# Optimization experiments

Measured on AMD Instinct MI355X. Metric: run time of the kernel, lower is better.

Reference implementation:

```python
import jax, jax.numpy as jnp
import numpy as np

N, NB, NP, T = 1024, 16, 256, 80
EPS_LEN = 1e-9   # seg_len clamp_min in original
EPS_DD = 1e-12   # dot(d,d) clamp_min in original


def setup_inputs() -> dict:
    key = jax.random.key(0)
    k1, k2, k3, k4 = jax.random.split(key, 4)
    # smooth-ish random trajectory (cumsum of steps)
    selected_traj = jnp.cumsum(jax.random.normal(k1, (N, T, 3), jnp.float32) * 0.5, axis=1)
    # random polylines per (sample, boundary)
    road_points = jnp.cumsum(jax.random.normal(k2, (N, NB, NP, 3), jnp.float32) * 0.5, axis=2) \
                  + jax.random.normal(k3, (N, NB, 1, 3), jnp.float32) * 2.0
    # ragged valid-prefix masks, length in [2, NP]
    lengths = jax.random.randint(k4, (N, NB), 2, NP + 1)
    road_mask = jnp.arange(NP)[None, None, :] < lengths[:, :, None]
    return {"selected_traj": selected_traj, "road_points": road_points, "road_mask": road_mask}


def _arc_project(pos, rp, rm):
    # pos: [N,T,3]; rp: [N,NB,NP,3]; rm: [N,NB,NP] bool
    n, t = pos.shape[0], pos.shape[1]
    nb, npts = rp.shape[1], rp.shape[2]
    inf = jnp.asarray(jnp.inf, pos.dtype)
    ar = jnp.arange(npts)
    n_valid = rm.sum(-1)                                    # [N,NB]

    # pack valid points to the front, preserving order (== boolean-mask gather in torch)
    order = jnp.argsort(jnp.logical_not(rm), axis=-1, stable=True)
    pts_f = jnp.take_along_axis(rp, order[..., None], axis=2)      # [N,NB,NP,3]
    pack_mask = ar[None, None, :] < n_valid[:, :, None]
    pts_f = jnp.where(pack_mask[..., None], pts_f, 0.0)
    # flipped direction: reverse the valid prefix
    flip_idx = jnp.clip(n_valid[:, :, None] - 1 - ar[None, None, :], 0, npts - 1)
    pts_b = jnp.take_along_axis(pts_f, flip_idx[..., None], axis=2)
    pts_b = jnp.where(pack_mask[..., None], pts_b, 0.0)
    pts = jnp.stack([pts_f, pts_b], axis=2)                 # [N,NB,2,NP,3]

    # segment i is real iff i < n_valid-1
    seg_mask = ar[: npts - 1][None, None, None, :] < (n_valid - 1)[:, :, None, None]  # [N,NB,1,NP-1]
    seg_vec = pts[..., 1:, :] - pts[..., :-1, :]            # [N,NB,2,NP-1,3]
    seg_norm = jnp.sqrt((seg_vec ** 2).sum(-1))
    seg_len = jnp.where(seg_mask, jnp.maximum(seg_norm, EPS_LEN), 0.0)
    cum_s = jnp.concatenate([jnp.zeros_like(seg_len[..., :1]), jnp.cumsum(seg_len, -1)], -1)  # [N,NB,2,NP]
    last_idx = jnp.clip(n_valid - 1, 0, npts - 1)[:, :, None, None]
    total_s = jnp.take_along_axis(cum_s, jnp.broadcast_to(last_idx, (n, nb, 2, 1)), -1)  # [N,NB,2,1]

    # entry: project first trajectory point onto nearest valid segment
    p0 = pos[:, 0][:, None, None, None, :]                  # [N,1,1,1,3]
    a0 = pts[..., :-1, :]
    dd0 = jnp.maximum((seg_vec ** 2).sum(-1), EPS_DD)
    t0 = jnp.clip(((p0 - a0) * seg_vec).sum(-1) / dd0, 0.0, 1.0)
    q0 = a0 + t0[..., None] * seg_vec
    d2 = jnp.where(seg_mask, ((p0 - q0) ** 2).sum(-1), inf)
    seg0 = jnp.argmin(d2, -1)[..., None]                    # [N,NB,2,1]
    entry_s = jnp.take_along_axis(cum_s, seg0, -1) + jnp.take_along_axis(t0 * seg_len, seg0, -1)

    # trajectory arc-length, resample polyline at entry_s + traj arc length
    traj_seg = jnp.sqrt(((pos[:, 1:] - pos[:, :-1]) ** 2).sum(-1))
    traj_cs = jnp.concatenate([jnp.zeros_like(traj_seg[:, :1]), jnp.cumsum(traj_seg, -1)], -1)  # [N,T]
    target_s = jnp.clip(entry_s + traj_cs[:, None, None, :], 0.0, total_s)  # [N,NB,2,T]

    j = jax.vmap(lambda c, tg: jnp.searchsorted(c, tg, side='right'))(
        cum_s.reshape(-1, npts), target_s.reshape(-1, t)) - 1
    j = jnp.clip(j.reshape(n, nb, 2, t), 0, jnp.maximum(n_valid[:, :, None, None] - 2, 0))

    seg_l = jnp.take_along_axis(seg_len, j, -1)
    cs_j = jnp.take_along_axis(cum_s, j, -1)
    t_loc = jnp.clip((target_s - cs_j) / jnp.maximum(seg_l, EPS_LEN), 0.0, 1.0)
    pa = jnp.take_along_axis(pts, j[..., None], axis=3)
    pb = jnp.take_along_axis(pts, (j + 1)[..., None], axis=3)
    proj = pa + t_loc[..., None] * (pb - pa)                # [N,NB,2,T,3]

    # pick (boundary, direction) candidate with min total L2 cost
    cost = jnp.sqrt(((pos[:, None, None] - proj) ** 2).sum(-1)).sum(-1)  # [N,NB,2]
    cand_ok = (n_valid >= 2)[:, :, None]
    cost = jnp.where(cand_ok, cost, inf)
    best = jnp.argmin(cost.reshape(n, -1), -1)
    best_proj = jnp.take_along_axis(proj.reshape(n, -1, t, 3), best[:, None, None, None], axis=1)[:, 0]
    has = cand_ok.any((1, 2))
    return jnp.where(has[:, None, None], best_proj, pos)


def reference(selected_traj, road_points, road_mask):
    pos = selected_traj[..., 0:3]
    out_pos = _arc_project(pos, road_points, road_mask)
    return jnp.concatenate([out_pos, selected_traj[..., 3:]], axis=-1)
```

## Files before the change

kernel.cpp:

```cpp
#include <hip/hip_runtime.h>
#include <math.h>

#define NN 1024
#define NBB 16
#define NP 256
#define TT 80
#define EPS_LEN 1e-9f
#define EPS_DD 1e-12f

__device__ __forceinline__ float frcp(float x){ return __builtin_amdgcn_rcpf(x); }
__device__ __forceinline__ float fsq(float x){ return __builtin_amdgcn_sqrtf(x); }
__device__ __forceinline__ float rfl_f(float x){
  return __builtin_bit_cast(float, __builtin_amdgcn_readfirstlane(__builtin_bit_cast(int, x)));
}
__device__ __forceinline__ float rlane_f(float x, int l){
  return __builtin_bit_cast(float, __builtin_amdgcn_readlane(__builtin_bit_cast(int, x), l));
}

template<int CTRL,int RM>
__device__ __forceinline__ float dpp_add(float v){
  int t = __builtin_amdgcn_update_dpp(0, __builtin_bit_cast(int, v), CTRL, RM, 0xf, true);
  return v + __builtin_bit_cast(float, t);
}
__device__ __forceinline__ float wave_incl_scan(float v){
  v = dpp_add<0x111,0xf>(v);
  v = dpp_add<0x112,0xf>(v);
  v = dpp_add<0x114,0xf>(v);
  v = dpp_add<0x118,0xf>(v);
  v = dpp_add<0x142,0xa>(v);
  v = dpp_add<0x143,0xc>(v);
  return v;
}
template<int CTRL,int RM>
__device__ __forceinline__ float dpp_min(float v){
  int t = __builtin_amdgcn_update_dpp(0x7f800000, __builtin_bit_cast(int,v), CTRL, RM, 0xf, false);
  return fminf(v, __builtin_bit_cast(float,t));
}
__device__ __forceinline__ float wave_min_all(float v){
  v=dpp_min<0x111,0xf>(v); v=dpp_min<0x112,0xf>(v);
  v=dpp_min<0x114,0xf>(v); v=dpp_min<0x118,0xf>(v);
  v=dpp_min<0x142,0xa>(v); v=dpp_min<0x143,0xc>(v);
  return rlane_f(v, 63);
}

__device__ __forceinline__ void lds_fence() {
  __builtin_amdgcn_wave_barrier();
  asm volatile("s_waitcnt lgkmcnt(0)" ::: "memory");
  __builtin_amdgcn_wave_barrier();
}

__device__ __forceinline__ int wave_nv(const void* mask, size_t base, int lane) {
  bool as_byte = ((const unsigned char*)mask)[1] != 0;
  int nv = 0;
  if (as_byte) {
    uchar4 v = ((const uchar4*)((const unsigned char*)mask + base))[lane];
    nv += __popcll(__ballot(v.x != 0));
    nv += __popcll(__ballot(v.y != 0));
    nv += __popcll(__ballot(v.z != 0));
    nv += __popcll(__ballot(v.w != 0));
  } else {
    int4 v = ((const int4*)((const int*)mask + base))[lane];
    nv += __popcll(__ballot(v.x != 0));
    nv += __popcll(__ballot(v.y != 0));
    nv += __popcll(__ballot(v.z != 0));
    nv += __popcll(__ballot(v.w != 0));
  }
  return nv;
}

template<bool STRICT>
__device__ __forceinline__ int count256(const float* __restrict__ cs,
                                        const float* co, float v){
  int K = 0;
  #pragma unroll
  for (int k=0;k<16;k++) K += STRICT ? (co[k] < v) : (co[k] <= v);
  int base = (K < 16 ? K : 15) * 16;
  const float4* f4 = (const float4*)(cs + base);
  float4 c0=f4[0], c1=f4[1], c2=f4[2], c3=f4[3];
  int r;
  if (STRICT)
    r = (c0.x<v)+(c0.y<v)+(c0.z<v)+(c0.w<v)+(c1.x<v)+(c1.y<v)+(c1.z<v)+(c1.w<v)
      + (c2.x<v)+(c2.y<v)+(c2.z<v)+(c2.w<v)+(c3.x<v)+(c3.y<v)+(c3.z<v)+(c3.w<v);
  else
    r = (c0.x<=v)+(c0.y<=v)+(c0.z<=v)+(c0.w<=v)+(c1.x<=v)+(c1.y<=v)+(c1.z<=v)+(c1.w<=v)
      + (c2.x<=v)+(c2.y<=v)+(c2.z<=v)+(c2.w<=v)+(c3.x<=v)+(c3.y<=v)+(c3.z<=v)+(c3.w<=v);
  return (K >= 16) ? 256 : (base + r);
}

struct SegOut {
  float cpre[4];
  float run;
  float bdf, btf; int bjf;
  float bdl, btl; int bjl;
};

__device__ __forceinline__ void seg_pass(const float4* __restrict__ p4, int lane, int nv,
                                         float p0x, float p0y, float p0z,
                                         float* __restrict__ px, float* __restrict__ py,
                                         float* __restrict__ pz, SegOut& R) {
  const int j0 = lane * 4;
  float4 A = make_float4(0.f,0.f,0.f,0.f), B = A, C = A;
  if (j0 < nv) { A = p4[lane*3+0]; B = p4[lane*3+1]; C = p4[lane*3+2]; }
  float x[5], y[5], z[5];
  x[0]=A.x; y[0]=A.y; z[0]=A.z;
  x[1]=A.w; y[1]=B.x; z[1]=B.y;
  x[2]=B.z; y[2]=B.w; z[2]=C.x;
  x[3]=C.y; y[3]=C.z; z[3]=C.w;
  x[4]=__shfl_down(x[0],1,64); y[4]=__shfl_down(y[0],1,64); z[4]=__shfl_down(z[0],1,64);
  ((float4*)px)[lane] = make_float4(x[0],x[1],x[2],x[3]);
  ((float4*)py)[lane] = make_float4(y[0],y[1],y[2],y[3]);
  ((float4*)pz)[lane] = make_float4(z[0],z[1],z[2],z[3]);
  float run = 0.f;
  R.bdf=INFINITY; R.btf=0.f; R.bjf=j0;
  R.bdl=INFINITY; R.btl=0.f; R.bjl=j0;
  #pragma unroll
  for (int k=0;k<4;k++){
    bool valid = (j0+k) < nv-1;
    float vx=x[k+1]-x[k], vy=y[k+1]-y[k], vz=z[k+1]-z[k];
    float n2 = vx*vx+vy*vy+vz*vz;
    float sl = valid ? fmaxf(fsq(n2), EPS_LEN) : 0.f;
    float t = ((p0x-x[k])*vx+(p0y-y[k])*vy+(p0z-z[k])*vz) * frcp(fmaxf(n2,EPS_DD));
    t = fminf(fmaxf(t,0.f),1.f);
    float qx=x[k]+t*vx, qy=y[k]+t*vy, qz=z[k]+t*vz;
    float dx=p0x-qx, dy=p0y-qy, dz=p0z-qz;
    float d2 = valid ? (dx*dx+dy*dy+dz*dz) : INFINITY;
    if (d2 <  R.bdf){R.bdf=d2; R.bjf=j0+k; R.btf=t;}
    if (d2 <= R.bdl){R.bdl=d2; R.bjl=j0+k; R.btl=t;}
    run += sl; R.cpre[k]=run;
  }
  R.run = run;
}

template<int MODE>
__device__ void eval_wave(float* __restrict__ px, float* __restrict__ py,
                          float* __restrict__ pz, float* __restrict__ cs,
                          const float* __restrict__ pos, const float* __restrict__ tc,
                          const float4* __restrict__ p4, int nv,
                          float* __restrict__ cost2, int wdir, float* __restrict__ out) {
  const int lane = threadIdx.x & 63;
  SegOut R;
  seg_pass(p4, lane, nv, pos[0], pos[1], pos[2], px, py, pz, R);

  float inc = wave_incl_scan(R.run);
  float ex = inc - R.run;
  ((float4*)cs)[lane] = make_float4(ex, ex+R.cpre[0], ex+R.cpre[1], ex+R.cpre[2]);

  const float Tot = rlane_f(inc, 63);

  float cval = ex + R.cpre[2];
  float co[16];
  #pragma unroll
  for (int k=0;k<16;k++) co[k] = rfl_f(__shfl(cval, 4*k+3, 64));

  float minv = wave_min_all(R.bdf);
  unsigned long long mf = __ballot(R.bdf == minv);
  unsigned long long ml = __ballot(R.bdl == minv);
  int lf = __builtin_ctzll(mf);
  int ll = 63 - __builtin_clzll(ml);
  int   jf = __builtin_amdgcn_readlane(R.bjf, lf);
  float tf = rlane_f(R.btf, lf);
  int   jl = __builtin_amdgcn_readlane(R.bjl, ll);
  float tl0 = rlane_f(R.btl, ll);

  constexpr int NPASS = (MODE==0)?3:2;
  float l_tc[NPASS];
  #pragma unroll
  for (int p=0;p<NPASS;p++){
    int task = p*64 + lane;
    int r = (MODE==0 && task>=TT) ? task-TT : task;
    int t = (r < TT) ? r : 0;
    l_tc[p] = tc[t];
  }

  lds_fence();

  float csjf = cs[jf], csjf1 = cs[jf+1];
  float csjl = cs[jl], csjl1 = cs[jl+1];
  float e0 = csjf + tf*(csjf1-csjf);
  float e1 = (Tot - csjl1) + (1.f-tl0)*(csjl1-csjl);

  const int jmaxv = nv-2;
  float accf=0.f, accr=0.f;
  #pragma unroll
  for (int p=0;p<NPASS;p++){
    int task = p*64 + lane;
    int dir, t; bool act;
    if (MODE==0){ act = task<2*TT; dir = task>=TT?1:0; t = dir ? task-TT : task; }
    else        { act = task<TT;   dir = wdir;         t = task; }
    float ts = (dir ? e1 : e0) + l_tc[p];
    ts = fminf(fmaxf(ts,0.f),Tot);
    int ia, ib; float tl;
    if (dir){
      float v = Tot - ts;
      int lb = count256<true>(cs, co, v);
      int j = nv-1-lb; j = j<0?0:(j>jmaxv?jmaxv:j);
      int l2 = nv-1-j;
      float base = Tot - cs[l2];
      tl = (ts-base)*frcp(fmaxf(cs[l2]-cs[l2-1], EPS_LEN));
      ia=l2; ib=l2-1;
    } else {
      int ub = count256<false>(cs, co, ts);
      int j = ub-1; j = j<0?0:(j>jmaxv?jmaxv:j);
      tl = (ts - cs[j])*frcp(fmaxf(cs[j+1]-cs[j], EPS_LEN));
      ia=j; ib=j+1;
    }
    tl = fminf(fmaxf(tl,0.f),1.f);
    float ax=px[ia], ay=py[ia], az=pz[ia];
    float bx=px[ib], by=py[ib], bz=pz[ib];
    float prx=ax+tl*(bx-ax), pry=ay+tl*(by-ay), prz=az+tl*(bz-az);
    if (MODE==1){
      if (act){ out[t*3+0]=prx; out[t*3+1]=pry; out[t*3+2]=prz; }
    } else if (act){
      float dx=pos[t*3+0]-prx, dy=pos[t*3+1]-pry, dz=pos[t*3+2]-prz;
      float dd=fsq(dx*dx+dy*dy+dz*dz);
      if (dir) accr+=dd; else accf+=dd;
    }
  }
  if (MODE==0){
    #pragma unroll
    for (int d=1;d<64;d<<=1){ accf+=__shfl_xor(accf,d,64); accr+=__shfl_xor(accr,d,64); }
    if (lane==0){ cost2[0]=accf; cost2[1]=accr; }
  }
}

__global__ __launch_bounds__(256)
void traj_cs_kernel(const float* __restrict__ traj, float* __restrict__ tcs) {
  const int wid = threadIdx.x>>6, lane = threadIdx.x&63;
  const int n = blockIdx.x*4 + wid;
  const float* p = traj + (size_t)n*TT*3;
  float* o = tcs + (size_t)n*TT;
  float dx=p[(lane+1)*3+0]-p[lane*3+0];
  float dy=p[(lane+1)*3+1]-p[lane*3+1];
  float dz=p[(lane+1)*3+2]-p[lane*3+2];
  float sA = sqrtf(dx*dx+dy*dy+dz*dz);
  float incA = sA;
  #pragma unroll
  for (int d=1;d<64;d<<=1){ float ov=__shfl_up(incA,d,64); if(lane>=d) incA+=ov; }
  o[lane+1] = incA;
  float tot = __shfl(incA, 63, 64);
  float sB = 0.f;
  if (lane<15){
    int t = 64+lane;
    float ex=p[(t+1)*3+0]-p[t*3+0];
    float ey=p[(t+1)*3+1]-p[t*3+1];
    float ez=p[(t+1)*3+2]-p[t*3+2];
    sB = sqrtf(ex*ex+ey*ey+ez*ez);
  }
  float incB = sB;
  #pragma unroll
  for (int d=1;d<64;d<<=1){ float ov=__shfl_up(incB,d,64); if(lane>=d) incB+=ov; }
  if (lane<15) o[65+lane] = tot + incB;
  if (lane==0) o[0] = 0.f;
}

__global__ __launch_bounds__(256, 8)
void fused_cost_kernel(const float* __restrict__ traj, const float* __restrict__ rp,
                       const void* __restrict__ mask, const float* __restrict__ tcs,
                       float* __restrict__ cost) {
  __shared__ float s_px[4][NP], s_py[4][NP], s_pz[4][NP], s_cs[4][NP];
  const int wid = threadIdx.x>>6, lane = threadIdx.x&63;
  const int nb = blockIdx.x*4 + wid;
  const int n = nb / NBB;
  int nvr = wave_nv(mask, (size_t)nb*NP, lane);
  if (nvr < 2){
    if (lane==0){ cost[nb*2+0]=INFINITY; cost[nb*2+1]=INFINITY; }
    return;
  }
  eval_wave<0>(s_px[wid],s_py[wid],s_pz[wid],s_cs[wid],
               traj+(size_t)n*TT*3, tcs+(size_t)n*TT,
               (const float4*)(rp+(size_t)nb*NP*3), nvr,
               cost+(size_t)nb*2, 0, nullptr);
}

__global__ __launch_bounds__(256)
void winner_kernel(const float* __restrict__ traj, const float* __restrict__ rp,
                   const void* __restrict__ mask, const float* __restrict__ tcs,
                   const float* __restrict__ cost, float* __restrict__ out) {
  __shared__ float s_px[4][NP], s_py[4][NP], s_pz[4][NP], s_cs[4][NP];
  const int wid = threadIdx.x>>6, lane = threadIdx.x&63;
  const int n = blockIdx.x*4 + wid;
  const float* c = cost + (size_t)n*NBB*2;
  float bc = (lane<NBB*2) ? c[lane] : INFINITY;
  int bi = (lane<NBB*2) ? lane : 64;
  #pragma unroll
  for (int d=1;d<64;d<<=1){
    float oc=__shfl_xor(bc,d,64); int oi=__shfl_xor(bi,d,64);
    if (oc<bc || (oc==bc && oi<bi)){bc=oc;bi=oi;}
  }
  const float* pos = traj + (size_t)n*TT*3;
  float* o = out + (size_t)n*TT*3;
  if (bc == INFINITY){
    if (lane < 60) ((float4*)o)[lane] = ((const float4*)pos)[lane];
    return;
  }
  int b = bi>>1, dir = bi&1;
  const size_t nbi = (size_t)n*NBB + b;
  int nv = wave_nv(mask, nbi*NP, lane);
  nv = max(nv, 2);
  eval_wave<1>(s_px[wid],s_py[wid],s_pz[wid],s_cs[wid],
               pos, tcs+(size_t)n*TT,
               (const float4*)(rp+nbi*NP*3), nv, nullptr, dir, o);
}

extern "C" void kernel_launch(void* const* d_in, const int* in_sizes, int n_in,
                              void* d_out, int out_size, void* d_ws, size_t ws_size,
                              hipStream_t stream) {
  const float* traj = (const float*)d_in[0];
  const float* rp   = (const float*)d_in[1];
  const void*  mask = d_in[2];
  float* tcs  = (float*)d_ws;
  float* cost = tcs + (size_t)NN * TT;
  float* out  = (float*)d_out;

  hipLaunchKernelGGL(traj_cs_kernel, dim3(NN/4), dim3(256), 0, stream, traj, tcs);
  hipLaunchKernelGGL(fused_cost_kernel, dim3(NN*NBB/4), dim3(256), 0, stream,
                     traj, rp, mask, tcs, cost);
  hipLaunchKernelGGL(winner_kernel, dim3(NN/4), dim3(256), 0, stream,
                     traj, rp, mask, tcs, cost, out);
}
```

Baseline: 35.66 us.

## Store entry arc positions from cost pass and skip min search in winner

The cost kernel now writes each candidate's forward and reverse entry arc-lengths to workspace. The winner kernel reads them back instead of recomputing the closest-segment search, so its segment pass drops the min-distance work. Points are stored interleaved xyz in LDS so each endpoint lookup is one float3 load. The entry cumsum values come from registers via readlane rather than LDS, and readfirstlane-of-shuffle becomes a direct readlane. The cost is an extra workspace array plus small global writes and reads.

```diff
diff --git a/kernel.cpp b/kernel.cpp
--- a/kernel.cpp
+++ b/kernel.cpp
@@ -10,9 +10,6 @@
 
 __device__ __forceinline__ float frcp(float x){ return __builtin_amdgcn_rcpf(x); }
 __device__ __forceinline__ float fsq(float x){ return __builtin_amdgcn_sqrtf(x); }
-__device__ __forceinline__ float rfl_f(float x){
-  return __builtin_bit_cast(float, __builtin_amdgcn_readfirstlane(__builtin_bit_cast(int, x)));
-}
 __device__ __forceinline__ float rlane_f(float x, int l){
   return __builtin_bit_cast(float, __builtin_amdgcn_readlane(__builtin_bit_cast(int, x), l));
 }
@@ -31,6 +28,7 @@
   v = dpp_add<0x143,0xc>(v);
   return v;
 }
+__device__ __forceinline__ float wave_sum(float v){ return rlane_f(wave_incl_scan(v), 63); }
 template<int CTRL,int RM>
 __device__ __forceinline__ float dpp_min(float v){
   int t = __builtin_amdgcn_update_dpp(0x7f800000, __builtin_bit_cast(int,v), CTRL, RM, 0xf, false);
@@ -94,10 +92,10 @@
   float bdl, btl; int bjl;
 };
 
+template<bool NEEDMIN>
 __device__ __forceinline__ void seg_pass(const float4* __restrict__ p4, int lane, int nv,
                                          float p0x, float p0y, float p0z,
-                                         float* __restrict__ px, float* __restrict__ py,
-                                         float* __restrict__ pz, SegOut& R) {
+                                         float* __restrict__ pts, SegOut& R) {
   const int j0 = lane * 4;
   float4 A = make_float4(0.f,0.f,0.f,0.f), B = A, C = A;
   if (j0 < nv) { A = p4[lane*3+0]; B = p4[lane*3+1]; C = p4[lane*3+2]; }
@@ -107,9 +105,9 @@
   x[2]=B.z; y[2]=B.w; z[2]=C.x;
   x[3]=C.y; y[3]=C.z; z[3]=C.w;
   x[4]=__shfl_down(x[0],1,64); y[4]=__shfl_down(y[0],1,64); z[4]=__shfl_down(z[0],1,64);
-  ((float4*)px)[lane] = make_float4(x[0],x[1],x[2],x[3]);
-  ((float4*)py)[lane] = make_float4(y[0],y[1],y[2],y[3]);
-  ((float4*)pz)[lane] = make_float4(z[0],z[1],z[2],z[3]);
+  ((float4*)pts)[lane*3+0] = make_float4(x[0],y[0],z[0],x[1]);
+  ((float4*)pts)[lane*3+1] = make_float4(y[1],z[1],x[2],y[2]);
+  ((float4*)pts)[lane*3+2] = make_float4(z[2],x[3],y[3],z[3]);
   float run = 0.f;
   R.bdf=INFINITY; R.btf=0.f; R.bjf=j0;
   R.bdl=INFINITY; R.btl=0.f; R.bjl=j0;
@@ -119,38 +117,82 @@
     float vx=x[k+1]-x[k], vy=y[k+1]-y[k], vz=z[k+1]-z[k];
     float n2 = vx*vx+vy*vy+vz*vz;
     float sl = valid ? fmaxf(fsq(n2), EPS_LEN) : 0.f;
-    float t = ((p0x-x[k])*vx+(p0y-y[k])*vy+(p0z-z[k])*vz) * frcp(fmaxf(n2,EPS_DD));
-    t = fminf(fmaxf(t,0.f),1.f);
-    float qx=x[k]+t*vx, qy=y[k]+t*vy, qz=z[k]+t*vz;
-    float dx=p0x-qx, dy=p0y-qy, dz=p0z-qz;
-    float d2 = valid ? (dx*dx+dy*dy+dz*dz) : INFINITY;
-    if (d2 <  R.bdf){R.bdf=d2; R.bjf=j0+k; R.btf=t;}
-    if (d2 <= R.bdl){R.bdl=d2; R.bjl=j0+k; R.btl=t;}
+    if (NEEDMIN){
+      float t = ((p0x-x[k])*vx+(p0y-y[k])*vy+(p0z-z[k])*vz) * frcp(fmaxf(n2,EPS_DD));
+      t = fminf(fmaxf(t,0.f),1.f);
+      float qx=x[k]+t*vx, qy=y[k]+t*vy, qz=z[k]+t*vz;
+      float dx=p0x-qx, dy=p0y-qy, dz=p0z-qz;
+      float d2 = valid ? (dx*dx+dy*dy+dz*dz) : INFINITY;
+      if (d2 <  R.bdf){R.bdf=d2; R.bjf=j0+k; R.btf=t;}
+      if (d2 <= R.bdl){R.bdl=d2; R.bjl=j0+k; R.btl=t;}
+    }
     run += sl; R.cpre[k]=run;
   }
   R.run = run;
 }
 
-template<int MODE>
-__device__ void eval_wave(float* __restrict__ px, float* __restrict__ py,
-                          float* __restrict__ pz, float* __restrict__ cs,
-                          const float* __restrict__ pos, const float* __restrict__ tc,
-                          const float4* __restrict__ p4, int nv,
-                          float* __restrict__ cost2, int wdir, float* __restrict__ out) {
+__device__ __forceinline__ void cs_pair_from_regs(int idx, float ex, const SegOut& R,
+                                                  float& c0, float& c1){
+  int o = idx >> 2, r = idx & 3;
+  float a0 = (r==0)?0.f : (r==1)?R.cpre[0] : (r==2)?R.cpre[1] : R.cpre[2];
+  float a1 = (r==0)?R.cpre[0] : (r==1)?R.cpre[1] : (r==2)?R.cpre[2] : R.run;
+  c0 = rlane_f(ex + a0, o);
+  c1 = rlane_f(ex + a1, o);
+}
+
+__device__ __forceinline__ void interp_at(const float* __restrict__ pts,
+                                          const float* __restrict__ cs,
+                                          const float* co, float Tot, int nv, int jmaxv,
+                                          int dir, float ts,
+                                          float& prx, float& pry, float& prz){
+  int ia, ib; float tl;
+  if (dir){
+    float v = Tot - ts;
+    int lb = count256<true>(cs, co, v);
+    int j = nv-1-lb; j = j<0?0:(j>jmaxv?jmaxv:j);
+    int l2 = nv-1-j;
+    float base = Tot - cs[l2];
+    tl = (ts-base)*frcp(fmaxf(cs[l2]-cs[l2-1], EPS_LEN));
+    ia=l2; ib=l2-1;
+  } else {
+    int ub = count256<false>(cs, co, ts);
+    int j = ub-1; j = j<0?0:(j>jmaxv?jmaxv:j);
+    tl = (ts - cs[j])*frcp(fmaxf(cs[j+1]-cs[j], EPS_LEN));
+    ia=j; ib=j+1;
+  }
+  tl = fminf(fmaxf(tl,0.f),1.f);
+  float3 PA = *(const float3*)(pts + ia*3);
+  float3 PB = *(const float3*)(pts + ib*3);
+  prx = PA.x + tl*(PB.x-PA.x);
+  pry = PA.y + tl*(PB.y-PA.y);
+  prz = PA.z + tl*(PB.z-PA.z);
+}
+
+__device__ void eval_cost_wave(float* __restrict__ pts, float* __restrict__ cs,
+                               const float* __restrict__ pos, const float* __restrict__ tc,
+                               const float4* __restrict__ p4, int nv,
+                               float* __restrict__ cost2, float2* __restrict__ ent2){
   const int lane = threadIdx.x & 63;
+  float l_tc[3];
+  #pragma unroll
+  for (int p=0;p<3;p++){
+    int task = p*64 + lane;
+    int r = task>=TT ? task-TT : task;
+    int t = (r<TT) ? r : 0;
+    l_tc[p] = tc[t];
+  }
   SegOut R;
-  seg_pass(p4, lane, nv, pos[0], pos[1], pos[2], px, py, pz, R);
+  seg_pass<true>(p4, lane, nv, pos[0], pos[1], pos[2], pts, R);
 
   float inc = wave_incl_scan(R.run);
   float ex = inc - R.run;
   ((float4*)cs)[lane] = make_float4(ex, ex+R.cpre[0], ex+R.cpre[1], ex+R.cpre[2]);
-
   const float Tot = rlane_f(inc, 63);
 
   float cval = ex + R.cpre[2];
   float co[16];
   #pragma unroll
-  for (int k=0;k<16;k++) co[k] = rfl_f(__shfl(cval, 4*k+3, 64));
+  for (int k=0;k<16;k++) co[k] = rlane_f(cval, 4*k+3);
 
   float minv = wave_min_all(R.bdf);
   unsigned long long mf = __ballot(R.bdf == minv);
@@ -162,64 +204,70 @@
   int   jl = __builtin_amdgcn_readlane(R.bjl, ll);
   float tl0 = rlane_f(R.btl, ll);
 
-  constexpr int NPASS = (MODE==0)?3:2;
-  float l_tc[NPASS];
-  #pragma unroll
-  for (int p=0;p<NPASS;p++){
-    int task = p*64 + lane;
-    int r = (MODE==0 && task>=TT) ? task-TT : task;
-    int t = (r < TT) ? r : 0;
-    l_tc[p] = tc[t];
-  }
+  float cjf, cjf1, cjl, cjl1;
+  cs_pair_from_regs(jf, ex, R, cjf, cjf1);
+  cs_pair_from_regs(jl, ex, R, cjl, cjl1);
+  float e0 = cjf + tf*(cjf1-cjf);
+  float e1 = (Tot - cjl1) + (1.f-tl0)*(cjl1-cjl);
 
   lds_fence();
-
-  float csjf = cs[jf], csjf1 = cs[jf+1];
-  float csjl = cs[jl], csjl1 = cs[jl+1];
-  float e0 = csjf + tf*(csjf1-csjf);
-  float e1 = (Tot - csjl1) + (1.f-tl0)*(csjl1-csjl);
 
   const int jmaxv = nv-2;
   float accf=0.f, accr=0.f;
   #pragma unroll
-  for (int p=0;p<NPASS;p++){
+  for (int p=0;p<3;p++){
     int task = p*64 + lane;
-    int dir, t; bool act;
-    if (MODE==0){ act = task<2*TT; dir = task>=TT?1:0; t = dir ? task-TT : task; }
-    else        { act = task<TT;   dir = wdir;         t = task; }
+    bool act = task < 2*TT;
+    int dir = task>=TT ? 1 : 0;
+    int t = dir ? task-TT : task;
     float ts = (dir ? e1 : e0) + l_tc[p];
     ts = fminf(fmaxf(ts,0.f),Tot);
-    int ia, ib; float tl;
-    if (dir){
-      float v = Tot - ts;
-      int lb = count256<true>(cs, co, v);
-      int j = nv-1-lb; j = j<0?0:(j>jmaxv?jmaxv:j);
-      int l2 = nv-1-j;
-      float base = Tot - cs[l2];
-      tl = (ts-base)*frcp(fmaxf(cs[l2]-cs[l2-1], EPS_LEN));
-      ia=l2; ib=l2-1;
-    } else {
-      int ub = count256<false>(cs, co, ts);
-      int j = ub-1; j = j<0?0:(j>jmaxv?jmaxv:j);
-      tl = (ts - cs[j])*frcp(fmaxf(cs[j+1]-cs[j], EPS_LEN));
-      ia=j; ib=j+1;
-    }
-    tl = fminf(fmaxf(tl,0.f),1.f);
-    float ax=px[ia], ay=py[ia], az=pz[ia];
-    float bx=px[ib], by=py[ib], bz=pz[ib];
-    float prx=ax+tl*(bx-ax), pry=ay+tl*(by-ay), prz=az+tl*(bz-az);
-    if (MODE==1){
-      if (act){ out[t*3+0]=prx; out[t*3+1]=pry; out[t*3+2]=prz; }
-    } else if (act){
+    float prx,pry,prz;
+    interp_at(pts, cs, co, Tot, nv, jmaxv, dir, ts, prx,pry,prz);
+    if (act){
       float dx=pos[t*3+0]-prx, dy=pos[t*3+1]-pry, dz=pos[t*3+2]-prz;
       float dd=fsq(dx*dx+dy*dy+dz*dz);
       if (dir) accr+=dd; else accf+=dd;
     }
   }
-  if (MODE==0){
-    #pragma unroll
-    for (int d=1;d<64;d<<=1){ accf+=__shfl_xor(accf,d,64); accr+=__shfl_xor(accr,d,64); }
-    if (lane==0){ cost2[0]=accf; cost2[1]=accr; }
+  float cf = wave_sum(accf), cr = wave_sum(accr);
+  if (lane==0){
+    cost2[0]=cf; cost2[1]=cr;
+    *ent2 = make_float2(e0, e1);
+  }
+}
+
+__device__ void eval_proj_wave(float* __restrict__ pts, float* __restrict__ cs,
+                               const float* __restrict__ tc,
+                               const float4* __restrict__ p4, int nv,
+                               int wdir, float entry, float* __restrict__ out){
+  const int lane = threadIdx.x & 63;
+  float l_tc[2];
+  #pragma unroll
+  for (int p=0;p<2;p++){
+    int t = p*64 + lane;
+    l_tc[p] = tc[(t<TT)?t:0];
+  }
+  SegOut R;
+  seg_pass<false>(p4, lane, nv, 0.f,0.f,0.f, pts, R);
+  float inc = wave_incl_scan(R.run);
+  float ex = inc - R.run;
+  ((float4*)cs)[lane] = make_float4(ex, ex+R.cpre[0], ex+R.cpre[1], ex+R.cpre[2]);
+  const float Tot = rlane_f(inc, 63);
+  float cval = ex + R.cpre[2];
+  float co[16];
+  #pragma unroll
+  for (int k=0;k<16;k++) co[k] = rlane_f(cval, 4*k+3);
+  lds_fence();
+  const int jmaxv = nv-2;
+  #pragma unroll
+  for (int p=0;p<2;p++){
+    int t = p*64 + lane;
+    float ts = entry + l_tc[p];
+    ts = fminf(fmaxf(ts,0.f),Tot);
+    float prx,pry,prz;
+    interp_at(pts, cs, co, Tot, nv, jmaxv, wdir, ts, prx,pry,prz);
+    if (t < TT){ out[t*3+0]=prx; out[t*3+1]=pry; out[t*3+2]=prz; }
   }
 }
 
@@ -256,8 +304,8 @@
 __global__ __launch_bounds__(256, 8)
 void fused_cost_kernel(const float* __restrict__ traj, const float* __restrict__ rp,
                        const void* __restrict__ mask, const float* __restrict__ tcs,
-                       float* __restrict__ cost) {
-  __shared__ float s_px[4][NP], s_py[4][NP], s_pz[4][NP], s_cs[4][NP];
+                       float* __restrict__ cost, float2* __restrict__ ent) {
+  __shared__ float s_pts[4][NP*3], s_cs[4][NP];
   const int wid = threadIdx.x>>6, lane = threadIdx.x&63;
   const int nb = blockIdx.x*4 + wid;
   const int n = nb / NBB;
@@ -266,17 +314,18 @@
     if (lane==0){ cost[nb*2+0]=INFINITY; cost[nb*2+1]=INFINITY; }
     return;
   }
-  eval_wave<0>(s_px[wid],s_py[wid],s_pz[wid],s_cs[wid],
-               traj+(size_t)n*TT*3, tcs+(size_t)n*TT,
-               (const float4*)(rp+(size_t)nb*NP*3), nvr,
-               cost+(size_t)nb*2, 0, nullptr);
+  eval_cost_wave(s_pts[wid], s_cs[wid],
+                 traj+(size_t)n*TT*3, tcs+(size_t)n*TT,
+                 (const float4*)(rp+(size_t)nb*NP*3), nvr,
+                 cost+(size_t)nb*2, ent+nb);
 }
 
 __global__ __launch_bounds__(256)
 void winner_kernel(const float* __restrict__ traj, const float* __restrict__ rp,
                    const void* __restrict__ mask, const float* __restrict__ tcs,
-                   const float* __restrict__ cost, float* __restrict__ out) {
-  __shared__ float s_px[4][NP], s_py[4][NP], s_pz[4][NP], s_cs[4][NP];
+                   const float* __restrict__ cost, const float2* __restrict__ ent,
+                   float* __restrict__ out) {
+  __shared__ float s_pts[4][NP*3], s_cs[4][NP];
   const int wid = threadIdx.x>>6, lane = threadIdx.x&63;
   const int n = blockIdx.x*4 + wid;
   const float* c = cost + (size_t)n*NBB*2;
@@ -295,11 +344,12 @@
   }
   int b = bi>>1, dir = bi&1;
   const size_t nbi = (size_t)n*NBB + b;
+  float2 eW = ent[nbi];
+  float entry = dir ? eW.y : eW.x;
   int nv = wave_nv(mask, nbi*NP, lane);
   nv = max(nv, 2);
-  eval_wave<1>(s_px[wid],s_py[wid],s_pz[wid],s_cs[wid],
-               pos, tcs+(size_t)n*TT,
-               (const float4*)(rp+nbi*NP*3), nv, nullptr, dir, o);
+  eval_proj_wave(s_pts[wid], s_cs[wid], tcs+(size_t)n*TT,
+                 (const float4*)(rp+nbi*NP*3), nv, dir, entry, o);
 }
 
 extern "C" void kernel_launch(void* const* d_in, const int* in_sizes, int n_in,
@@ -310,11 +360,12 @@
   const void*  mask = d_in[2];
   float* tcs  = (float*)d_ws;
   float* cost = tcs + (size_t)NN * TT;
+  float2* ent = (float2*)(cost + (size_t)NN*NBB*2);
   float* out  = (float*)d_out;
 
   hipLaunchKernelGGL(traj_cs_kernel, dim3(NN/4), dim3(256), 0, stream, traj, tcs);
   hipLaunchKernelGGL(fused_cost_kernel, dim3(NN*NBB/4), dim3(256), 0, stream,
-                     traj, rp, mask, tcs, cost);
+                     traj, rp, mask, tcs, cost, ent);
   hipLaunchKernelGGL(winner_kernel, dim3(NN/4), dim3(256), 0, stream,
-                     traj, rp, mask, tcs, cost, out);
-}
+                     traj, rp, mask, tcs, cost, ent, out);
+}
```

Measured after the change: 34.91 us. -2.1%, faster.
